# Kernel tuning notes

Measured on AMD Instinct MI355X. Metric: run time of the kernel, lower is better.

## Reference

```python
import jax, jax.numpy as jnp
import numpy as np

N = 197          # tokens (== token_count)
B = 64           # batch
D = 768          # d_model
NH = 12          # n_head
GH = 2           # global_heads
HR = NH // GH    # head_ratio = 6
DH = 64          # d_head
QK = GH * DH     # qk_dim = 128
ML = 3           # mask_levels
EPS = 1e-5


def setup_inputs() -> dict:
    key = jax.random.key(0)
    ks = jax.random.split(key, 9)
    s = 1.0 / np.sqrt(D)
    return {
        "h": jax.random.normal(ks[0], (N, B, D), dtype=jnp.float32),
        "masks": jax.random.uniform(ks[1], (N, N, ML), dtype=jnp.float32),
        "Wq": jax.random.normal(ks[2], (QK, D), dtype=jnp.float32) * s,
        "Wk": jax.random.normal(ks[3], (QK, D), dtype=jnp.float32) * s,
        "Wv": jax.random.normal(ks[4], (NH * DH, D), dtype=jnp.float32) * s,
        "Wo": jax.random.normal(ks[5], (D, NH * DH), dtype=jnp.float32) * s,
        "mask_proj": jnp.ones((ML, NH), dtype=jnp.float32),
        "ln_gamma": jnp.ones((D,), dtype=jnp.float32),
        "ln_beta": jnp.zeros((D,), dtype=jnp.float32),
    }


def reference(h, masks, Wq, Wk, Wv, Wo, mask_proj, ln_gamma, ln_beta):
    scale = 1.0 / np.sqrt(DH)
    # projections (seq-first layout [N, B, ...])
    q = (h @ Wq.T).reshape(N, B, GH, DH)
    k = (h @ Wk.T).reshape(N, B, GH, DH)
    v = (h @ Wv.T).reshape(N, B, NH, DH)
    # global-head scores: [B, GH, i, j]
    score = jnp.einsum('ibgd,jbgd->bgij', q, k) * scale
    # learned mask mix: [i, j, NH] -> [GH, i, j, HR] (g-major head split, matches torch reshape)
    mw = jnp.einsum('ijl,ln->ijn', masks, mask_proj)
    mw = mw.reshape(N, N, GH, HR).transpose(2, 0, 1, 3)
    # broadcast each global head to HR local heads: [B, GH, i, j, HR]
    attn = score[..., None] * mw[None]
    attn = attn.transpose(0, 1, 4, 2, 3).reshape(B, NH, N, N)  # head = g*HR + r
    prob = jax.nn.softmax(attn, axis=-1)
    # AV: [i, B, NH, DH] -> [N, B, NH*DH]
    vec = jnp.einsum('bnij,jbnd->ibnd', prob, v).reshape(N, B, NH * DH)
    out = vec @ Wo.T
    # post-LN residual
    x = h + out
    mu = jnp.mean(x, axis=-1, keepdims=True)
    var = jnp.var(x, axis=-1, keepdims=True)
    return ln_gamma * (x - mu) / jnp.sqrt(var + EPS) + ln_beta
```

## Files before the change

### kernel.cpp

```cpp
#include <hip/hip_runtime.h>
#include <hip/hip_bf16.h>
#include <stdint.h>

#define NTOK 197
#define NPAD 224
#define BATCH 64
#define DMODEL 768
#define NHEAD 12
#define GHEAD 2
#define HRATIO 6
#define DHEAD 64
#define QKDIM 128
#define LNEPS 1e-5f
#define MROWS (NTOK * BATCH)
#define MPAD 12672

using f32x4 = __attribute__((ext_vector_type(4))) float;
using s16x8 = __attribute__((ext_vector_type(8))) short;
using s16x4 = __attribute__((ext_vector_type(4))) short;

__device__ __forceinline__ short f2bf(float f) {
  unsigned int x = __float_as_uint(f);
  return (short)((x + 0x7fffu + ((x >> 16) & 1u)) >> 16);
}

__device__ __forceinline__ float bf2f(short s) {
  return __uint_as_float((unsigned)(unsigned short)s << 16);
}

__device__ __forceinline__ void gld16(void* lds, const void* g) {
  __builtin_amdgcn_global_load_lds(
      (const __attribute__((address_space(1))) unsigned int*)g,
      (__attribute__((address_space(3))) unsigned int*)lds, 16, 0, 0);
}

#define NB_H 4728
#define NB_QKV 384
#define NB_WO 288
__global__ __launch_bounds__(256)
void prep_kernel(const float* __restrict__ h, const float* __restrict__ Wq,
                 const float* __restrict__ Wk, const float* __restrict__ Wv,
                 const float* __restrict__ Wo, short* __restrict__ hb,
                 short* __restrict__ Wqkvb, short* __restrict__ Wob) {
  const int bb = blockIdx.x, t = threadIdx.x;
  const float* src;
  short* dst;
  if (bb < NB_H) {
    int idx = bb * 256 + t;
    src = h + (size_t)idx * 8;
    dst = hb + (size_t)idx * 8;
  } else if (bb < NB_H + NB_QKV) {
    int idx = (bb - NB_H) * 256 + t;
    int r = idx / 96, u = idx - r * 96;
    const float* s0 = (r < 128) ? Wq + (size_t)r * DMODEL
                    : (r < 256) ? Wk + (size_t)(r - 128) * DMODEL
                                : Wv + (size_t)(r - 256) * DMODEL;
    src = s0 + u * 8;
    dst = Wqkvb + (size_t)r * DMODEL + u * 8;
  } else {
    int idx = (bb - NB_H - NB_QKV) * 256 + t;
    src = Wo + (size_t)idx * 8;
    dst = Wob + (size_t)idx * 8;
  }
  float4 a = *(const float4*)src;
  float4 c = *(const float4*)(src + 4);
  s16x8 o;
  o[0] = f2bf(a.x); o[1] = f2bf(a.y); o[2] = f2bf(a.z); o[3] = f2bf(a.w);
  o[4] = f2bf(c.x); o[5] = f2bf(c.y); o[6] = f2bf(c.z); o[7] = f2bf(c.w);
  *(s16x8*)dst = o;
}

__global__ __launch_bounds__(256)
void gemm_bt_kernel(const short* __restrict__ A, const short* __restrict__ W,
                    short* __restrict__ Cout, int M, int K, int NC) {
  __shared__ short As[128 * 32];
  __shared__ short Ws[128 * 32];
  const int tid = threadIdx.x;

  const int nwg = gridDim.x * gridDim.y;
  const int orig = blockIdx.y * gridDim.x + blockIdx.x;
  const int qq = nwg >> 3, rr = nwg & 7;
  const int xcd = orig & 7, sidx = orig >> 3;
  const int wg = (xcd < rr ? xcd * (qq + 1) : rr * (qq + 1) + (xcd - rr) * qq) + sidx;
  const int bn = (wg % gridDim.x) * 128;
  const int bm = (wg / gridDim.x) * 128;

  const int w = tid >> 6, l = tid & 63;
  const int wr = w >> 1, wc = w & 1;
  const int lm = l & 15, lh = l >> 4;

  const int srow = tid >> 2;
  const int schunk = (tid & 3) ^ ((tid >> 3) & 3);
  const short* Ag = A + (size_t)(bm + srow) * K + schunk * 8;
  const short* Wg = W + (size_t)(bn + srow) * K + schunk * 8;

  const int csw = lh ^ ((lm >> 1) & 3);
  f32x4 acc[4][4] = {};

  for (int kt = 0; kt < K; kt += 32) {
    __syncthreads();
    gld16(As + tid * 8, Ag + kt);
    gld16(As + 2048 + tid * 8, Ag + (size_t)64 * K + kt);
    gld16(Ws + tid * 8, Wg + kt);
    gld16(Ws + 2048 + tid * 8, Wg + (size_t)64 * K + kt);
    __syncthreads();
    s16x8 af[4], bf[4];
#pragma unroll
    for (int m = 0; m < 4; ++m)
      af[m] = *(const s16x8*)((const char*)As + (wr * 64 + m * 16 + lm) * 64 + csw * 16);
#pragma unroll
    for (int n = 0; n < 4; ++n)
      bf[n] = *(const s16x8*)((const char*)Ws + (wc * 64 + n * 16 + lm) * 64 + csw * 16);
#pragma unroll
    for (int m = 0; m < 4; ++m)
#pragma unroll
      for (int n = 0; n < 4; ++n)
        acc[m][n] = __builtin_amdgcn_mfma_f32_16x16x32_bf16(af[m], bf[n], acc[m][n], 0, 0, 0);
  }

#pragma unroll
  for (int m = 0; m < 4; ++m) {
#pragma unroll
    for (int r = 0; r < 4; ++r) {
      int row = bm + wr * 64 + m * 16 + lh * 4 + r;
      if (row < M) {
#pragma unroll
        for (int n = 0; n < 4; ++n) {
          int col = bn + wc * 64 + n * 16 + lm;
          Cout[(size_t)row * NC + col] = f2bf(acc[m][n][r]);
        }
      }
    }
  }
}

__global__ __launch_bounds__(256)
void packall_kernel(const short* __restrict__ Cb, const float* __restrict__ masks,
                    const float* __restrict__ mproj, short* __restrict__ qp,
                    short* __restrict__ kp, short* __restrict__ vT,
                    float* __restrict__ mwp) {
  __shared__ short Vs[NPAD][DHEAD + 1];
  const int bb = blockIdx.x, t = threadIdx.x;
  if (bb < 256) {
    int b = bb >> 2, g = (bb >> 1) & 1, which = bb & 1;
    short* dst = (which ? kp : qp) + ((size_t)b * GHEAD + g) * NPAD * 64;
    int d = t & 63, iofs = t >> 6;
    for (int i0 = 0; i0 < NPAD; i0 += 4) {
      int i = i0 + iofs;
      short v = 0;
      if (i < NTOK)
        v = Cb[(size_t)(i * BATCH + b) * 1024 + which * QKDIM + g * DHEAD + d];
      int dd = which ? ((((d >> 3) ^ (i & 7)) << 3) | (d & 7)) : d;
      dst[i * 64 + dd] = v;
    }
  } else if (bb < 1024) {
    int vv = bb - 256;
    int b = vv / 12, n = vv - b * 12;
    int d = t & 63, iofs = t >> 6;
    for (int i0 = 0; i0 < NPAD; i0 += 4) {
      int i = i0 + iofs;
      short v = 0;
      if (i < NTOK)
        v = Cb[(size_t)(i * BATCH + b) * 1024 + 256 + n * DHEAD + d];
      Vs[i][d] = v;
    }
    __syncthreads();
    short* dst = vT + ((size_t)b * NHEAD + n) * DHEAD * NPAD;
    int sub = t & 63, dr = t >> 6;
    for (int d0 = 0; d0 < DHEAD; d0 += 4) {
      if (sub < 56) {
        int dd = d0 + dr, j0 = sub * 4;
        s16x4 o;
        o[0] = Vs[j0][dd]; o[1] = Vs[j0 + 1][dd];
        o[2] = Vs[j0 + 2][dd]; o[3] = Vs[j0 + 3][dd];
        *(s16x4*)(dst + dd * NPAD + j0) = o;
      }
    }
  } else {
    int e = (bb - 1024) * 256 + t;
    int n = e >> 12;
    int rem = e & 4095;
    int i = rem >> 4, lm = rem & 15;
    float p0 = mproj[n], p1 = mproj[NHEAD + n], p2 = mproj[2 * NHEAD + n];
    float vals[16];
#pragma unroll
    for (int jf = 0; jf < 16; ++jf) vals[jf] = 0.f;
    if (i < NTOK) {
#pragma unroll
      for (int jf = 0; jf < 14; ++jf) {
        int col = jf * 16 + lm;
        if (col < NTOK) {
          const float* mp = masks + ((size_t)i * NTOK + col) * 3;
          vals[jf] = 0.125f * (mp[0] * p0 + mp[1] * p1 + mp[2] * p2);
        }
      }
    }
    float* dst = mwp + (size_t)e * 16;
#pragma unroll
    for (int q = 0; q < 4; ++q) {
      float4 o = make_float4(vals[q * 4], vals[q * 4 + 1], vals[q * 4 + 2], vals[q * 4 + 3]);
      *(float4*)(dst + q * 4) = o;
    }
  }
}

__global__ __launch_bounds__(256, 2)
void attn_fused_kernel(const short* __restrict__ qp, const short* __restrict__ kp,
                       const short* __restrict__ vT, const float* __restrict__ mwp,
                       short* __restrict__ vec_b) {
  const int it = blockIdx.x, b = blockIdx.y, g = blockIdx.z;
  __shared__ short Ks[NPAD * 64];
  __shared__ short Pt[64 * 256];
  __shared__ float rsb[64];
  const int t = threadIdx.x, w = t >> 6, l = t & 63;
  const int lm = l & 15, lh = l >> 4, l7 = l & 7;

  const short* qg = qp + ((size_t)b * GHEAD + g) * NPAD * 64;
  const short* kg = kp + ((size_t)b * GHEAD + g) * NPAD * 64;

#pragma unroll
  for (int s = 0; s < 7; ++s)
    gld16(Ks + s * 2048 + t * 8, kg + s * 2048 + t * 8);
  int qrow = it * 64 + w * 16 + lm;
  if (qrow > NPAD - 1) qrow = NPAD - 1;
  s16x8 a0 = *(const s16x8*)(qg + qrow * 64 + lh * 8);
  s16x8 a1 = *(const s16x8*)(qg + qrow * 64 + 32 + lh * 8);
  __syncthreads();

  f32x4 acc[14] = {};
#pragma unroll
  for (int jf = 0; jf < 14; ++jf) {
    s16x8 kf0 = *(const s16x8*)((const char*)Ks + (jf * 16 + lm) * 128 + ((lh ^ l7) << 4));
    s16x8 kf1 = *(const s16x8*)((const char*)Ks + (jf * 16 + lm) * 128 + (((4 + lh) ^ l7) << 4));
    acc[jf] = __builtin_amdgcn_mfma_f32_16x16x32_bf16(a0, kf0, acc[jf], 0, 0, 0);
    acc[jf] = __builtin_amdgcn_mfma_f32_16x16x32_bf16(a1, kf1, acc[jf], 0, 0, 0);
  }

  for (int hh = 0; hh < HRATIO; ++hh) {
    const int n = g * HRATIO + hh;
    const short* vg = vT + ((size_t)b * NHEAD + n) * 64 * NPAD;
    s16x8 vf[7];
#pragma unroll
    for (int ks = 0; ks < 7; ++ks)
      vf[ks] = *(const s16x8*)(vg + (w * 16 + lm) * NPAD + ks * 32 + lh * 8);

#pragma unroll
    for (int r = 0; r < 4; ++r) {
      const int row = w * 16 + lh * 4 + r;
      const int i = it * 64 + row;
      const float* mr = mwp + (((size_t)n * 256 + i) * 16 + lm) * 16;
      f32x4 mv0 = *(const f32x4*)(mr);
      f32x4 mv1 = *(const f32x4*)(mr + 4);
      f32x4 mv2 = *(const f32x4*)(mr + 8);
      f32x4 mv3 = *(const f32x4*)(mr + 12);
      float sum = 0.f;
#pragma unroll
      for (int jf = 0; jf < 13; ++jf) {
        float mwv = (jf < 4) ? mv0[jf] : (jf < 8) ? mv1[jf - 4]
                  : (jf < 12) ? mv2[jf - 8] : mv3[jf - 12];
        float pe = __expf(acc[jf][r] * mwv);
        if (jf == 12 && lm >= 5) pe = 0.f;
        sum += pe;
        int byteoff = row * 512 + (((2 * jf + (lm >> 3)) ^ (row & 7)) << 4) + (lm & 7) * 2;
        *(short*)((char*)Pt + byteoff) = f2bf(pe);
      }
      {
        int byteoff = row * 512 + (((26 + (lm >> 3)) ^ (row & 7)) << 4) + (lm & 7) * 2;
        *(short*)((char*)Pt + byteoff) = 0;
      }
#pragma unroll
      for (int off = 8; off; off >>= 1) sum += __shfl_xor(sum, off);
      if (lm == 0) rsb[row] = 1.f / sum;
    }
    __syncthreads();

    __builtin_amdgcn_s_setprio(1);
    f32x4 oacc[4] = {};
#pragma unroll
    for (int fi = 0; fi < 4; ++fi)
#pragma unroll
      for (int ks = 0; ks < 7; ++ks) {
        s16x8 pa = *(const s16x8*)((const char*)Pt + (fi * 16 + lm) * 512 +
                                   (((ks * 4 + lh) ^ l7) << 4));
        oacc[fi] = __builtin_amdgcn_mfma_f32_16x16x32_bf16(pa, vf[ks], oacc[fi], 0, 0, 0);
      }
    __builtin_amdgcn_s_setprio(0);
#pragma unroll
    for (int fi = 0; fi < 4; ++fi)
#pragma unroll
      for (int r = 0; r < 4; ++r) {
        int ia = it * 64 + fi * 16 + lh * 4 + r;
        if (ia < NTOK) {
          float rsv = rsb[fi * 16 + lh * 4 + r];
          vec_b[((size_t)ia * BATCH + b) * DMODEL + n * 64 + w * 16 + lm] =
              f2bf(oacc[fi][r] * rsv);
        }
      }
    __syncthreads();
  }
}

__global__ __launch_bounds__(256)
void ln_kernel(const float* __restrict__ h, const short* __restrict__ proj_b,
               float* __restrict__ out, const float* __restrict__ gamma,
               const float* __restrict__ beta) {
  const int m = blockIdx.x;
  const float* hrow = h + (size_t)m * DMODEL;
  const short* prow = proj_b + (size_t)m * DMODEL;
  float* orow = out + (size_t)m * DMODEL;
  const int tid = threadIdx.x;
  float v0 = hrow[tid] + bf2f(prow[tid]);
  float v1 = hrow[tid + 256] + bf2f(prow[tid + 256]);
  float v2 = hrow[tid + 512] + bf2f(prow[tid + 512]);
  float s = v0 + v1 + v2;
  float sq = v0 * v0 + v1 * v1 + v2 * v2;
#pragma unroll
  for (int off = 32; off; off >>= 1) {
    s += __shfl_xor(s, off);
    sq += __shfl_xor(sq, off);
  }
  __shared__ float ss[4], ssq[4];
  const int w = tid >> 6, lane = tid & 63;
  if (lane == 0) { ss[w] = s; ssq[w] = sq; }
  __syncthreads();
  s = ss[0] + ss[1] + ss[2] + ss[3];
  sq = ssq[0] + ssq[1] + ssq[2] + ssq[3];
  const float inv = 1.0f / (float)DMODEL;
  float mu = s * inv;
  float var = sq * inv - mu * mu;
  float rstd = rsqrtf(var + LNEPS);
  orow[tid] = gamma[tid] * (v0 - mu) * rstd + beta[tid];
  orow[tid + 256] = gamma[tid + 256] * (v1 - mu) * rstd + beta[tid + 256];
  orow[tid + 512] = gamma[tid + 512] * (v2 - mu) * rstd + beta[tid + 512];
}

extern "C" void kernel_launch(void* const* d_in, const int* in_sizes, int n_in,
                              void* d_out, int out_size, void* d_ws, size_t ws_size,
                              hipStream_t stream) {
  const float* h     = (const float*)d_in[0];
  const float* masks = (const float*)d_in[1];
  const float* Wq    = (const float*)d_in[2];
  const float* Wk    = (const float*)d_in[3];
  const float* Wv    = (const float*)d_in[4];
  const float* Wo    = (const float*)d_in[5];
  const float* mproj = (const float*)d_in[6];
  const float* gamma = (const float*)d_in[7];
  const float* beta  = (const float*)d_in[8];
  float* out = (float*)d_out;

  char* ws = (char*)d_ws;
  size_t o = 0;
  auto alloc = [&](size_t bytes) { size_t r = o; o += (bytes + 255) & ~(size_t)255; return r; };
  short* hb    = (short*)(ws + alloc((size_t)MPAD * DMODEL * 2));
  short* Cb    = (short*)(ws + alloc((size_t)MPAD * 1024 * 2));
  short* Wqkvb = (short*)(ws + alloc((size_t)1024 * DMODEL * 2));
  short* Wob   = (short*)(ws + alloc((size_t)DMODEL * DMODEL * 2));
  short* qp    = (short*)(ws + alloc((size_t)BATCH * GHEAD * NPAD * DHEAD * 2));
  short* kp    = (short*)(ws + alloc((size_t)BATCH * GHEAD * NPAD * DHEAD * 2));
  short* vT    = (short*)(ws + alloc((size_t)BATCH * NHEAD * DHEAD * NPAD * 2));
  float* mwp   = (float*)(ws + alloc((size_t)NHEAD * 256 * 16 * 16 * 4));
  short* vec_b = hb;
  short* proj_b = Cb;

  prep_kernel<<<NB_H + NB_QKV + NB_WO, 256, 0, stream>>>(h, Wq, Wk, Wv, Wo, hb, Wqkvb, Wob);
  gemm_bt_kernel<<<dim3(1024 / 128, MPAD / 128), 256, 0, stream>>>(
      hb, Wqkvb, Cb, MROWS, DMODEL, 1024);
  packall_kernel<<<1216, 256, 0, stream>>>(Cb, masks, mproj, qp, kp, vT, mwp);
  attn_fused_kernel<<<dim3(4, BATCH, GHEAD), 256, 0, stream>>>(qp, kp, vT, mwp, vec_b);
  gemm_bt_kernel<<<dim3(DMODEL / 128, MPAD / 128), 256, 0, stream>>>(
      vec_b, Wob, proj_b, MROWS, DMODEL, DMODEL);
  ln_kernel<<<MROWS, 256, 0, stream>>>(h, proj_b, out, gamma, beta);
}
```

Baseline: 156.0 us.

## Double-buffer LDS tiles in bf16 GEMM to overlap global loads with MFMA

Replaces the single-buffered LDS staging in the GEMM kernel with two buffers, issuing the global-to-LDS loads for the next K tile before computing on the current one. Explicit waitcnt and barrier instructions replace __syncthreads to order the buffer swaps. The aim is to hide global load latency behind MFMA work, at the cost of doubling LDS usage per block, which may lower occupancy.

```diff
diff --git a/kernel.cpp b/kernel.cpp
--- a/kernel.cpp
+++ b/kernel.cpp
@@ -73,8 +73,8 @@
 __global__ __launch_bounds__(256)
 void gemm_bt_kernel(const short* __restrict__ A, const short* __restrict__ W,
                     short* __restrict__ Cout, int M, int K, int NC) {
-  __shared__ short As[128 * 32];
-  __shared__ short Ws[128 * 32];
+  __shared__ short As[2 * 128 * 32];
+  __shared__ short Ws[2 * 128 * 32];
   const int tid = threadIdx.x;
 
   const int nwg = gridDim.x * gridDim.y;
@@ -97,26 +97,39 @@
   const int csw = lh ^ ((lm >> 1) & 3);
   f32x4 acc[4][4] = {};
 
-  for (int kt = 0; kt < K; kt += 32) {
-    __syncthreads();
-    gld16(As + tid * 8, Ag + kt);
-    gld16(As + 2048 + tid * 8, Ag + (size_t)64 * K + kt);
-    gld16(Ws + tid * 8, Wg + kt);
-    gld16(Ws + 2048 + tid * 8, Wg + (size_t)64 * K + kt);
-    __syncthreads();
+#define STAGE(buf, kt)                                              \
+  do {                                                              \
+    gld16(As + (buf) * 4096 + tid * 8, Ag + (kt));                  \
+    gld16(As + (buf) * 4096 + 2048 + tid * 8, Ag + (size_t)64 * K + (kt)); \
+    gld16(Ws + (buf) * 4096 + tid * 8, Wg + (kt));                  \
+    gld16(Ws + (buf) * 4096 + 2048 + tid * 8, Wg + (size_t)64 * K + (kt)); \
+  } while (0)
+
+  const int NK = K >> 5;
+  STAGE(0, 0);
+  for (int ki = 0; ki < NK; ++ki) {
+    const int cur = ki & 1;
+    asm volatile("s_waitcnt vmcnt(0)" ::: "memory");
+    __builtin_amdgcn_s_barrier();
+    if (ki + 1 < NK) STAGE(cur ^ 1, (ki + 1) * 32);
+    const char* Ab = (const char*)(As + cur * 4096);
+    const char* Bb = (const char*)(Ws + cur * 4096);
     s16x8 af[4], bf[4];
 #pragma unroll
     for (int m = 0; m < 4; ++m)
-      af[m] = *(const s16x8*)((const char*)As + (wr * 64 + m * 16 + lm) * 64 + csw * 16);
+      af[m] = *(const s16x8*)(Ab + (wr * 64 + m * 16 + lm) * 64 + csw * 16);
 #pragma unroll
     for (int n = 0; n < 4; ++n)
-      bf[n] = *(const s16x8*)((const char*)Ws + (wc * 64 + n * 16 + lm) * 64 + csw * 16);
+      bf[n] = *(const s16x8*)(Bb + (wc * 64 + n * 16 + lm) * 64 + csw * 16);
 #pragma unroll
     for (int m = 0; m < 4; ++m)
 #pragma unroll
       for (int n = 0; n < 4; ++n)
         acc[m][n] = __builtin_amdgcn_mfma_f32_16x16x32_bf16(af[m], bf[n], acc[m][n], 0, 0, 0);
-  }
+    asm volatile("s_waitcnt lgkmcnt(0)" ::: "memory");
+    __builtin_amdgcn_s_barrier();
+  }
+#undef STAGE
 
 #pragma unroll
   for (int m = 0; m < 4; ++m) {
```

Measured after the change: 151.2 us. 1.03x faster.

## Pre-swizzle GEMM operands into MFMA fragment layout and load directly to registers

Applied to the files above, without the earlier changes.

The prep kernel now writes h, Wqkv and Wo in a blocked layout that matches the MFMA operand fragments (128-row bands by 32-wide k chunks). The GEMM then reads fragments straight from global memory into registers with double-buffering, with no LDS staging and no __syncthreads. The attention kernel writes its output directly in this fragment layout so the output-projection GEMM can consume it. This removes LDS traffic and barriers, at the cost of complex index arithmetic and no on-chip reuse between waves sharing A or B tiles, which relies on L2/L1 instead.

```diff
diff --git a/kernel.cpp b/kernel.cpp
--- a/kernel.cpp
+++ b/kernel.cpp
@@ -14,6 +14,8 @@
 #define LNEPS 1e-5f
 #define MROWS (NTOK * BATCH)
 #define MPAD 12672
+#define NKC 24
+#define NBAND 99
 
 using f32x4 = __attribute__((ext_vector_type(4))) float;
 using s16x8 = __attribute__((ext_vector_type(8))) short;
@@ -34,99 +36,115 @@
       (__attribute__((address_space(3))) unsigned int*)lds, 16, 0, 0);
 }
 
-#define NB_H 4728
-#define NB_QKV 384
-#define NB_WO 288
+#define NBH (NBAND * NKC)
+#define NBQ (8 * NKC)
+#define NBW (6 * NKC)
 __global__ __launch_bounds__(256)
 void prep_kernel(const float* __restrict__ h, const float* __restrict__ Wq,
                  const float* __restrict__ Wk, const float* __restrict__ Wv,
-                 const float* __restrict__ Wo, short* __restrict__ hb,
-                 short* __restrict__ Wqkvb, short* __restrict__ Wob) {
+                 const float* __restrict__ Wo, short* __restrict__ hf,
+                 short* __restrict__ Wqkvf, short* __restrict__ Wof) {
   const int bb = blockIdx.x, t = threadIdx.x;
-  const float* src;
-  short* dst;
-  if (bb < NB_H) {
-    int idx = bb * 256 + t;
-    src = h + (size_t)idx * 8;
-    dst = hb + (size_t)idx * 8;
-  } else if (bb < NB_H + NB_QKV) {
-    int idx = (bb - NB_H) * 256 + t;
-    int r = idx / 96, u = idx - r * 96;
-    const float* s0 = (r < 128) ? Wq + (size_t)r * DMODEL
-                    : (r < 256) ? Wk + (size_t)(r - 128) * DMODEL
-                                : Wv + (size_t)(r - 256) * DMODEL;
-    src = s0 + u * 8;
-    dst = Wqkvb + (size_t)r * DMODEL + u * 8;
-  } else {
-    int idx = (bb - NB_H - NB_QKV) * 256 + t;
-    src = Wo + (size_t)idx * 8;
-    dst = Wob + (size_t)idx * 8;
-  }
-  float4 a = *(const float4*)src;
-  float4 c = *(const float4*)(src + 4);
-  s16x8 o;
-  o[0] = f2bf(a.x); o[1] = f2bf(a.y); o[2] = f2bf(a.z); o[3] = f2bf(a.w);
-  o[4] = f2bf(c.x); o[5] = f2bf(c.y); o[6] = f2bf(c.z); o[7] = f2bf(c.w);
-  *(s16x8*)dst = o;
+  int band, kc, which;
+  if (bb < NBH) { which = 0; band = bb / NKC; kc = bb - band * NKC; }
+  else if (bb < NBH + NBQ) { int i = bb - NBH; which = 1; band = i / NKC; kc = i - band * NKC; }
+  else { int i = bb - NBH - NBQ; which = 2; band = i / NKC; kc = i - band * NKC; }
+  short* dstS = (which == 0 ? hf : which == 1 ? Wqkvf : Wof) +
+                ((size_t)(band * NKC + kc) * 8) * 512;
+#pragma unroll
+  for (int uu = 0; uu < 2; ++uu) {
+    int u = t + uu * 256;
+    int frag = u >> 6, l = u & 63;
+    int rl = frag * 16 + (l & 15);
+    int k0 = kc * 32 + ((l >> 4) & 3) * 8;
+    float4 a = {0, 0, 0, 0}, c = {0, 0, 0, 0};
+    if (which == 0) {
+      int row = band * 128 + rl;
+      if (row < MROWS) {
+        const float* p = h + (size_t)row * DMODEL + k0;
+        a = *(const float4*)p; c = *(const float4*)(p + 4);
+      }
+    } else if (which == 1) {
+      int row = band * 128 + rl;
+      const float* src = (row < 128) ? Wq + (size_t)row * DMODEL
+                       : (row < 256) ? Wk + (size_t)(row - 128) * DMODEL
+                                     : Wv + (size_t)(row - 256) * DMODEL;
+      a = *(const float4*)(src + k0); c = *(const float4*)(src + k0 + 4);
+    } else {
+      const float* p = Wo + (size_t)(band * 128 + rl) * DMODEL + k0;
+      a = *(const float4*)p; c = *(const float4*)(p + 4);
+    }
+    s16x8 o;
+    o[0] = f2bf(a.x); o[1] = f2bf(a.y); o[2] = f2bf(a.z); o[3] = f2bf(a.w);
+    o[4] = f2bf(c.x); o[5] = f2bf(c.y); o[6] = f2bf(c.z); o[7] = f2bf(c.w);
+    *(s16x8*)(dstS + (size_t)u * 8) = o;
+  }
 }
 
 __global__ __launch_bounds__(256)
-void gemm_bt_kernel(const short* __restrict__ A, const short* __restrict__ W,
-                    short* __restrict__ Cout, int M, int K, int NC) {
-  __shared__ short As[128 * 32];
-  __shared__ short Ws[128 * 32];
+void gemm_frag_kernel(const short* __restrict__ Af, const short* __restrict__ Bf,
+                      short* __restrict__ Cout, int M, int NC) {
   const int tid = threadIdx.x;
-
   const int nwg = gridDim.x * gridDim.y;
   const int orig = blockIdx.y * gridDim.x + blockIdx.x;
   const int qq = nwg >> 3, rr = nwg & 7;
   const int xcd = orig & 7, sidx = orig >> 3;
   const int wg = (xcd < rr ? xcd * (qq + 1) : rr * (qq + 1) + (xcd - rr) * qq) + sidx;
-  const int bn = (wg % gridDim.x) * 128;
-  const int bm = (wg / gridDim.x) * 128;
+  const int cb = wg % gridDim.x;
+  const int rb = wg / gridDim.x;
 
   const int w = tid >> 6, l = tid & 63;
   const int wr = w >> 1, wc = w & 1;
   const int lm = l & 15, lh = l >> 4;
 
-  const int srow = tid >> 2;
-  const int schunk = (tid & 3) ^ ((tid >> 3) & 3);
-  const short* Ag = A + (size_t)(bm + srow) * K + schunk * 8;
-  const short* Wg = W + (size_t)(bn + srow) * K + schunk * 8;
-
-  const int csw = lh ^ ((lm >> 1) & 3);
+  const short* pa = Af + ((size_t)(rb * NKC) * 8 + wr * 4) * 512 + l * 8;
+  const short* pb = Bf + ((size_t)(cb * NKC) * 8 + wc * 4) * 512 + l * 8;
+
   f32x4 acc[4][4] = {};
-
-  for (int kt = 0; kt < K; kt += 32) {
-    __syncthreads();
-    gld16(As + tid * 8, Ag + kt);
-    gld16(As + 2048 + tid * 8, Ag + (size_t)64 * K + kt);
-    gld16(Ws + tid * 8, Wg + kt);
-    gld16(Ws + 2048 + tid * 8, Wg + (size_t)64 * K + kt);
-    __syncthreads();
-    s16x8 af[4], bf[4];
-#pragma unroll
-    for (int m = 0; m < 4; ++m)
-      af[m] = *(const s16x8*)((const char*)As + (wr * 64 + m * 16 + lm) * 64 + csw * 16);
-#pragma unroll
-    for (int n = 0; n < 4; ++n)
-      bf[n] = *(const s16x8*)((const char*)Ws + (wc * 64 + n * 16 + lm) * 64 + csw * 16);
-#pragma unroll
-    for (int m = 0; m < 4; ++m)
-#pragma unroll
-      for (int n = 0; n < 4; ++n)
-        acc[m][n] = __builtin_amdgcn_mfma_f32_16x16x32_bf16(af[m], bf[n], acc[m][n], 0, 0, 0);
-  }
+  s16x8 A0[4], B0[4], A1[4], B1[4];
+
+#define LOADF(Ar, Br, kc)                                   \
+  do {                                                      \
+    const short* qa = pa + (size_t)(kc) * 4096;             \
+    const short* qb = pb + (size_t)(kc) * 4096;             \
+    Ar[0] = *(const s16x8*)(qa);                            \
+    Ar[1] = *(const s16x8*)(qa + 512);                      \
+    Ar[2] = *(const s16x8*)(qa + 1024);                     \
+    Ar[3] = *(const s16x8*)(qa + 1536);                     \
+    Br[0] = *(const s16x8*)(qb);                            \
+    Br[1] = *(const s16x8*)(qb + 512);                      \
+    Br[2] = *(const s16x8*)(qb + 1024);                     \
+    Br[3] = *(const s16x8*)(qb + 1536);                     \
+  } while (0)
+
+#define MM(Ar, Br)                                                             \
+  do {                                                                         \
+    _Pragma("unroll") for (int m = 0; m < 4; ++m)                              \
+      _Pragma("unroll") for (int n = 0; n < 4; ++n)                            \
+        acc[m][n] = __builtin_amdgcn_mfma_f32_16x16x32_bf16(Ar[m], Br[n],      \
+                                                            acc[m][n], 0, 0, 0);\
+  } while (0)
+
+  LOADF(A0, B0, 0);
+#pragma unroll
+  for (int kc = 0; kc < NKC; kc += 2) {
+    LOADF(A1, B1, kc + 1);
+    MM(A0, B0);
+    if (kc + 2 < NKC) LOADF(A0, B0, kc + 2);
+    MM(A1, B1);
+  }
+#undef LOADF
+#undef MM
 
 #pragma unroll
   for (int m = 0; m < 4; ++m) {
 #pragma unroll
     for (int r = 0; r < 4; ++r) {
-      int row = bm + wr * 64 + m * 16 + lh * 4 + r;
+      int row = rb * 128 + wr * 64 + m * 16 + lh * 4 + r;
       if (row < M) {
 #pragma unroll
         for (int n = 0; n < 4; ++n) {
-          int col = bn + wc * 64 + n * 16 + lm;
+          int col = cb * 128 + wc * 64 + n * 16 + lm;
           Cout[(size_t)row * NC + col] = f2bf(acc[m][n][r]);
         }
       }
@@ -207,7 +225,7 @@
 __global__ __launch_bounds__(256, 2)
 void attn_fused_kernel(const short* __restrict__ qp, const short* __restrict__ kp,
                        const short* __restrict__ vT, const float* __restrict__ mwp,
-                       short* __restrict__ vec_b) {
+                       short* __restrict__ vec_f) {
   const int it = blockIdx.x, b = blockIdx.y, g = blockIdx.z;
   __shared__ short Ks[NPAD * 64];
   __shared__ short Pt[64 * 256];
@@ -235,6 +253,9 @@
     acc[jf] = __builtin_amdgcn_mfma_f32_16x16x32_bf16(a0, kf0, acc[jf], 0, 0, 0);
     acc[jf] = __builtin_amdgcn_mfma_f32_16x16x32_bf16(a1, kf1, acc[jf], 0, 0, 0);
   }
+
+  const int b4 = b >> 4;
+  const int lofs = ((((w & 1) << 1) + (lm >> 3)) * 16 + (b & 15)) * 8 + (lm & 7);
 
   for (int hh = 0; hh < HRATIO; ++hh) {
     const int n = g * HRATIO + hh;
@@ -285,6 +306,7 @@
         oacc[fi] = __builtin_amdgcn_mfma_f32_16x16x32_bf16(pa, vf[ks], oacc[fi], 0, 0, 0);
       }
     __builtin_amdgcn_s_setprio(0);
+    const int kcH = n * 2 + (w >> 1);
 #pragma unroll
     for (int fi = 0; fi < 4; ++fi)
 #pragma unroll
@@ -292,8 +314,9 @@
         int ia = it * 64 + fi * 16 + lh * 4 + r;
         if (ia < NTOK) {
           float rsv = rsb[fi * 16 + lh * 4 + r];
-          vec_b[((size_t)ia * BATCH + b) * DMODEL + n * 64 + w * 16 + lm] =
-              f2bf(oacc[fi][r] * rsv);
+          int fragidx = ((it * 32 + fi * 8 + lh * 2 + (r >> 1)) * NKC + kcH) * 8 +
+                        ((r & 1) << 2) + b4;
+          vec_f[(size_t)fragidx * 512 + lofs] = f2bf(oacc[fi][r] * rsv);
         }
       }
     __syncthreads();
@@ -351,23 +374,21 @@
   char* ws = (char*)d_ws;
   size_t o = 0;
   auto alloc = [&](size_t bytes) { size_t r = o; o += (bytes + 255) & ~(size_t)255; return r; };
-  short* hb    = (short*)(ws + alloc((size_t)MPAD * DMODEL * 2));
+  short* hf    = (short*)(ws + alloc((size_t)MPAD * DMODEL * 2));
   short* Cb    = (short*)(ws + alloc((size_t)MPAD * 1024 * 2));
-  short* Wqkvb = (short*)(ws + alloc((size_t)1024 * DMODEL * 2));
-  short* Wob   = (short*)(ws + alloc((size_t)DMODEL * DMODEL * 2));
+  short* Wqkvf = (short*)(ws + alloc((size_t)1024 * DMODEL * 2));
+  short* Wof   = (short*)(ws + alloc((size_t)DMODEL * DMODEL * 2));
   short* qp    = (short*)(ws + alloc((size_t)BATCH * GHEAD * NPAD * DHEAD * 2));
   short* kp    = (short*)(ws + alloc((size_t)BATCH * GHEAD * NPAD * DHEAD * 2));
   short* vT    = (short*)(ws + alloc((size_t)BATCH * NHEAD * DHEAD * NPAD * 2));
   float* mwp   = (float*)(ws + alloc((size_t)NHEAD * 256 * 16 * 16 * 4));
-  short* vec_b = hb;
+  short* vec_f = hf;
   short* proj_b = Cb;
 
-  prep_kernel<<<NB_H + NB_QKV + NB_WO, 256, 0, stream>>>(h, Wq, Wk, Wv, Wo, hb, Wqkvb, Wob);
-  gemm_bt_kernel<<<dim3(1024 / 128, MPAD / 128), 256, 0, stream>>>(
-      hb, Wqkvb, Cb, MROWS, DMODEL, 1024);
+  prep_kernel<<<NBH + NBQ + NBW, 256, 0, stream>>>(h, Wq, Wk, Wv, Wo, hf, Wqkvf, Wof);
+  gemm_frag_kernel<<<dim3(8, NBAND), 256, 0, stream>>>(hf, Wqkvf, Cb, MROWS, 1024);
   packall_kernel<<<1216, 256, 0, stream>>>(Cb, masks, mproj, qp, kp, vT, mwp);
-  attn_fused_kernel<<<dim3(4, BATCH, GHEAD), 256, 0, stream>>>(qp, kp, vT, mwp, vec_b);
-  gemm_bt_kernel<<<dim3(DMODEL / 128, MPAD / 128), 256, 0, stream>>>(
-      vec_b, Wob, proj_b, MROWS, DMODEL, DMODEL);
+  attn_fused_kernel<<<dim3(4, BATCH, GHEAD), 256, 0, stream>>>(qp, kp, vT, mwp, vec_f);
+  gemm_frag_kernel<<<dim3(6, NBAND), 256, 0, stream>>>(vec_f, Wof, proj_b, MROWS, DMODEL);
   ln_kernel<<<MROWS, 256, 0, stream>>>(h, proj_b, out, gamma, beta);
 }
```

New measurement: 144.1 us. -7.6%, faster.
